# Kernel optimization log

Measured on AMD Instinct MI355X. Metric: run time of the kernel, lower is better.

## Reference

```python
import jax, jax.numpy as jnp
import numpy as np

B, T, N, IN, H, P = 1, 48, 4096, 2, 64, 12


def _normalize_adj(adj):
    A = adj + jnp.eye(adj.shape[0], dtype=adj.dtype)
    d = jnp.sum(A, axis=1)
    dinv = jnp.where(d > 0, d ** -0.5, 0.0)
    return (dinv[:, None] * A) * dinv[None, :]


def _cell(inp, h, c, A, gcWi, gcbi, gcWh, gcbh, liWi, libi, liWh, libh):
    # graph conv: spmm(A, inp @ W) + bias, plus plain linears; all produce [BN, 4H]
    comb = (A @ (inp @ gcWi) + gcbi
            + A @ (h @ gcWh) + gcbh
            + inp @ liWi + libi
            + h @ liWh + libh)
    i_g, f_g, o_g, g_g = jnp.split(comb, 4, axis=1)
    new_c = jax.nn.sigmoid(f_g) * c + jax.nn.sigmoid(i_g) * jnp.tanh(g_g)
    new_h = jax.nn.sigmoid(o_g) * jnp.tanh(new_c)
    return new_h, new_c


def setup_inputs() -> dict:
    key = jax.random.key(0)
    ks = jax.random.split(key, 24)
    s_in = 1.0 / np.sqrt(4 * H)

    def p(k, shape):
        return jax.random.normal(k, shape, dtype=jnp.float32) * s_in

    adj = (jax.random.uniform(ks[1], (N, N)) < 0.01).astype(jnp.float32)
    return {
        "x": jax.random.normal(ks[0], (B, T, N * IN), dtype=jnp.float32),
        "adj": adj,
        "gcWi0": p(ks[2], (IN, 4 * H)), "gcbi0": p(ks[3], (4 * H,)),
        "gcWh0": p(ks[4], (H, 4 * H)), "gcbh0": p(ks[5], (4 * H,)),
        "liWi0": p(ks[6], (IN, 4 * H)), "libi0": p(ks[7], (4 * H,)),
        "liWh0": p(ks[8], (H, 4 * H)), "libh0": p(ks[9], (4 * H,)),
        "gcWi1": p(ks[10], (H, 4 * H)), "gcbi1": p(ks[11], (4 * H,)),
        "gcWh1": p(ks[12], (H, 4 * H)), "gcbh1": p(ks[13], (4 * H,)),
        "liWi1": p(ks[14], (H, 4 * H)), "libi1": p(ks[15], (4 * H,)),
        "liWh1": p(ks[16], (H, 4 * H)), "libh1": p(ks[17], (4 * H,)),
        "outW": p(ks[18], (H, P)), "outb": p(ks[19], (P,)),
    }


def reference(x, adj, gcWi0, gcbi0, gcWh0, gcbh0, liWi0, libi0, liWh0, libh0,
              gcWi1, gcbi1, gcWh1, gcbh1, liWi1, libi1, liWh1, libh1, outW, outb):
    A = _normalize_adj(adj)
    # [B,T,N*IN] -> time-major [T, B*N, IN]
    xs = x.reshape(B, T, N, IN).transpose(1, 0, 2, 3).reshape(T, B * N, IN)
    z = jnp.zeros((B * N, H), dtype=x.dtype)

    def step(carry, xt):
        h0, c0, h1, c1 = carry
        h0, c0 = _cell(xt, h0, c0, A, gcWi0, gcbi0, gcWh0, gcbh0,
                       liWi0, libi0, liWh0, libh0)
        # dropout is identity in eval mode
        h1, c1 = _cell(h0, h1, c1, A, gcWi1, gcbi1, gcWh1, gcbh1,
                       liWi1, libi1, liWh1, libh1)
        return (h0, c0, h1, c1), None

    (h0, c0, h1, c1), _ = jax.lax.scan(step, (z, z, z, z), xs)
    out = h1 @ outW + outb  # [B*N, P]
    return out.reshape(B, N, P)
```

## Files before the change

### kernel.cpp

```cpp
#include <hip/hip_runtime.h>
#include <math.h>

#define NN 4096
#define TT 48
#define HH 64
#define GG 256
#define PP 12
#define CAP 192
#define NH (NN * HH)

__device__ __forceinline__ float bcast_f(float v, int lane) {
  return __int_as_float(__builtin_amdgcn_readlane(__float_as_int(v), lane));
}
__device__ __forceinline__ int bcast_i(int v, int lane) {
  return __builtin_amdgcn_readlane(v, lane);
}

__launch_bounds__(256)
__global__ void k_prep(const float* gcbi0, const float* gcbh0,
                       const float* libi0, const float* libh0,
                       const float* gcbi1, const float* gcbh1,
                       const float* libi1, const float* libh1,
                       const float* gcWh0, const float* liWh0,
                       const float* gcWi1, const float* liWi1,
                       const float* gcWh1, const float* liWh1,
                       const float* gcWi0, const float* liWi0,
                       float* state, float4* Wg0, float4* Wg1,
                       float4* biasg0, float4* biasg1, float4* xq0) {
  int idx = blockIdx.x * 256 + threadIdx.x;
  int stride = gridDim.x * 256;
  for (int i = idx; i < 6 * NH; i += stride) state[i] = 0.0f;
  for (int i = idx; i < 64 * 2 * 64; i += stride) {
    int j = i & 63, m = (i >> 6) & 1, k = i >> 7;
    const float* W = m ? liWh0 : gcWh0;
    Wg0[i] = make_float4(W[k * GG + j], W[k * GG + j + 64],
                         W[k * GG + j + 128], W[k * GG + j + 192]);
  }
  for (int i = idx; i < 64 * 4 * 64; i += stride) {
    int j = i & 63, m = (i >> 6) & 3, k = i >> 8;
    const float* W = (m == 0) ? gcWi1 : (m == 1) ? liWi1 : (m == 2) ? gcWh1 : liWh1;
    Wg1[i] = make_float4(W[k * GG + j], W[k * GG + j + 64],
                         W[k * GG + j + 128], W[k * GG + j + 192]);
  }
  if (idx < 64) {
    int j = idx;
    biasg0[j] = make_float4(
        gcbi0[j] + gcbh0[j] + libi0[j] + libh0[j],
        gcbi0[j + 64] + gcbh0[j + 64] + libi0[j + 64] + libh0[j + 64],
        gcbi0[j + 128] + gcbh0[j + 128] + libi0[j + 128] + libh0[j + 128],
        gcbi0[j + 192] + gcbh0[j + 192] + libi0[j + 192] + libh0[j + 192]);
    biasg1[j] = make_float4(
        gcbi1[j] + gcbh1[j] + libi1[j] + libh1[j],
        gcbi1[j + 64] + gcbh1[j + 64] + libi1[j + 64] + libh1[j + 64],
        gcbi1[j + 128] + gcbh1[j + 128] + libi1[j + 128] + libh1[j + 128],
        gcbi1[j + 192] + gcbh1[j + 192] + libi1[j + 192] + libh1[j + 192]);
  } else if (idx < 320) {
    int i = idx - 64;
    int j = i & 63, m = i >> 6;
    const float* W = (m < 2) ? gcWi0 : liWi0;
    int kk = m & 1;
    xq0[i] = make_float4(W[kk * GG + j], W[kk * GG + j + 64],
                         W[kk * GG + j + 128], W[kk * GG + j + 192]);
  }
}

__launch_bounds__(256)
__global__ void k_build(const float* adj, float* dinv,
                        int* ell_col, float* ell_val, int* ell_cnt) {
  int r = blockIdx.x;
  __shared__ int cnt;
  __shared__ float red[256];
  if (threadIdx.x == 0) cnt = 0;
  __syncthreads();
  const float* row = adj + (size_t)r * NN;
  float s = 0.0f;
  for (int c = threadIdx.x; c < NN; c += 256) {
    float a = row[c];
    if (c == r) a += 1.0f;
    s += a;
    if (a != 0.0f) {
      int pos = atomicAdd(&cnt, 1);
      if (pos < CAP) {
        ell_col[(size_t)r * CAP + pos] = c;
        ell_val[(size_t)r * CAP + pos] = a;
      }
    }
  }
  red[threadIdx.x] = s;
  __syncthreads();
  for (int st = 128; st > 0; st >>= 1) {
    if (threadIdx.x < st) red[threadIdx.x] += red[threadIdx.x + st];
    __syncthreads();
  }
  int n = cnt < CAP ? cnt : CAP;
  for (int j = n + (int)threadIdx.x; j < CAP; j += 256) {
    ell_col[(size_t)r * CAP + j] = 0;
    ell_val[(size_t)r * CAP + j] = 0.0f;
  }
  if (threadIdx.x == 0) {
    int npad = (n + 7) & ~7;
    if (npad > CAP) npad = CAP;
    ell_cnt[r] = npad;
    dinv[r] = 1.0f / sqrtf(red[0]);
  }
}

__launch_bounds__(256)
__global__ void k_scale(const float* dinv, const int* ell_col, float* ell_val) {
  int idx = blockIdx.x * 256 + threadIdx.x;
  int r = idx / CAP;
  if (r >= NN) return;
  float v = ell_val[idx];
  if (v != 0.0f) ell_val[idx] = v * dinv[r] * dinv[ell_col[idx]];
}

__launch_bounds__(256)
__global__ void k_gax(const float* x, const int* ell_col, const float* ell_val,
                      const int* ell_cnt, float* gax) {
  int t = blockIdx.x >> 3;
  int seg = blockIdx.x & 7;
  __shared__ float xs[NN * 2];
  const float* xt = x + (size_t)t * NN * 2;
  for (int i = threadIdx.x; i < NN * 2; i += 256) xs[i] = xt[i];
  __syncthreads();
  int base = seg * 512 * 2;
  for (int oo = threadIdx.x; oo < 512 * 2; oo += 256) {
    int o = base + oo;
    int r = o >> 1, cmp = o & 1;
    int cnt = ell_cnt[r];
    const int* cp = ell_col + (size_t)r * CAP;
    const float* vp = ell_val + (size_t)r * CAP;
    float acc = 0.0f;
    for (int j = 0; j < cnt; j += 4) {
      acc += vp[j]     * xs[cp[j]     * 2 + cmp];
      acc += vp[j + 1] * xs[cp[j + 1] * 2 + cmp];
      acc += vp[j + 2] * xs[cp[j + 2] * 2 + cmp];
      acc += vp[j + 3] * xs[cp[j + 3] * 2 + cmp];
    }
    gax[(size_t)t * NN * 2 + o] = acc;
  }
}

__launch_bounds__(256)
__global__ void k_cells(int c0on, int c1on,
                        const int* __restrict__ ell_col,
                        const float* __restrict__ ell_val,
                        const int* __restrict__ ell_cnt,
                        const float2* __restrict__ Pr, float* __restrict__ Pw,
                        float* __restrict__ c0, float* __restrict__ c1,
                        const float* __restrict__ xt, const float* __restrict__ gaxt,
                        const float4* __restrict__ Wg,
                        const float4* __restrict__ biasg0,
                        const float4* __restrict__ xq0,
                        const float4* __restrict__ biasg1) {
  __shared__ float4 wbuf[2048];
  const int tid = threadIdx.x;
  const int wave = tid >> 6, lane = tid & 63;
  const int r0 = blockIdx.x * 8 + wave * 2;

  const float4* pf = Wg + tid;
  float4 st0 = pf[0], st1 = pf[256], st2 = pf[512], st3 = pf[768];
  pf += 1024;

  float cprev0[2], cprev1[2];
#pragma unroll
  for (int rr = 0; rr < 2; rr++) {
    size_t gi = (size_t)(r0 + rr) * HH + lane;
    cprev0[rr] = c0[gi];
    cprev1[rr] = c1[gi];
  }

  int myc[2][3]; float myv[2][3]; int cnts[2];
#pragma unroll
  for (int rr = 0; rr < 2; rr++) {
    int r = r0 + rr;
    cnts[rr] = ell_cnt[r];
#pragma unroll
    for (int chk = 0; chk < 3; chk++) {
      myc[rr][chk] = ell_col[(size_t)r * CAP + chk * 64 + lane];
      myv[rr][chk] = ell_val[(size_t)r * CAP + chk * 64 + lane];
    }
  }

  float ga0[2], ga1[2], hl0[2], hl1[2];
#pragma unroll
  for (int rr = 0; rr < 2; rr++) {
    int cnt = cnts[rr];
    float a0 = 0.0f, a1 = 0.0f;
#pragma unroll
    for (int chk = 0; chk < 3; chk++) {
      int base = chk * 64;
      if (base < cnt) {
        int lim = cnt - base; if (lim > 64) lim = 64;
        int mc = myc[rr][chk]; float mv = myv[rr][chk];
        for (int m = 0; m < lim; m += 8) {
          float2 ld[8]; float vv[8];
#pragma unroll
          for (int i = 0; i < 8; i++) {
            int cc = bcast_i(mc, m + i);
            vv[i] = bcast_f(mv, m + i);
            ld[i] = Pr[(size_t)cc * 64 + lane];
          }
#pragma unroll
          for (int i = 0; i < 8; i++) {
            a0 += vv[i] * ld[i].x;
            a1 += vv[i] * ld[i].y;
          }
        }
      }
    }
    ga0[rr] = a0;
    ga1[rr] = a1;
    float2 hh = Pr[(size_t)(r0 + rr) * 64 + lane];
    hl0[rr] = hh.x;
    hl1[rr] = hh.y;
  }

  float4 acc0[2], acc1[2];
  {
    float4 b = biasg0[lane];
    float4 qg0 = xq0[lane], qg1 = xq0[64 + lane];
    float4 ql0 = xq0[128 + lane], ql1 = xq0[192 + lane];
#pragma unroll
    for (int rr = 0; rr < 2; rr++) {
      float xx0 = xt[(size_t)(r0 + rr) * 2];
      float xx1 = xt[(size_t)(r0 + rr) * 2 + 1];
      float gg0 = gaxt[(size_t)(r0 + rr) * 2];
      float gg1 = gaxt[(size_t)(r0 + rr) * 2 + 1];
      acc0[rr].x = b.x + gg0 * qg0.x + gg1 * qg1.x + xx0 * ql0.x + xx1 * ql1.x;
      acc0[rr].y = b.y + gg0 * qg0.y + gg1 * qg1.y + xx0 * ql0.y + xx1 * ql1.y;
      acc0[rr].z = b.z + gg0 * qg0.z + gg1 * qg1.z + xx0 * ql0.z + xx1 * ql1.z;
      acc0[rr].w = b.w + gg0 * qg0.w + gg1 * qg1.w + xx0 * ql0.w + xx1 * ql1.w;
    }
    float4 b1 = biasg1[lane];
    acc1[0] = b1; acc1[1] = b1;
  }

  wbuf[tid] = st0; wbuf[256 + tid] = st1;
  wbuf[512 + tid] = st2; wbuf[768 + tid] = st3;
  __syncthreads();
  int cur = 0;

#pragma unroll 1
  for (int ch = 0; ch < 8; ch++) {
    st0 = pf[0]; st1 = pf[256]; st2 = pf[512]; st3 = pf[768];
    pf += 1024;
    const float4* wb = wbuf + (cur << 10);
#pragma unroll
    for (int kk = 0; kk < 8; kk++) {
      int k = ch * 8 + kk;
      float4 w0 = wb[(kk * 2 + 0) * 64 + lane];
      float4 w1 = wb[(kk * 2 + 1) * 64 + lane];
#pragma unroll
      for (int rr = 0; rr < 2; rr++) {
        float a0 = bcast_f(ga0[rr], k);
        float a1 = bcast_f(hl0[rr], k);
        acc0[rr].x += a0 * w0.x + a1 * w1.x;
        acc0[rr].y += a0 * w0.y + a1 * w1.y;
        acc0[rr].z += a0 * w0.z + a1 * w1.z;
        acc0[rr].w += a0 * w0.w + a1 * w1.w;
      }
    }
    cur ^= 1;
    float4* dst = wbuf + (cur << 10) + tid;
    dst[0] = st0; dst[256] = st1; dst[512] = st2; dst[768] = st3;
    __syncthreads();
  }

  if (c0on) {
#pragma unroll
    for (int rr = 0; rr < 2; rr++) {
      size_t gi = (size_t)(r0 + rr) * HH + lane;
      float si = 1.0f / (1.0f + __expf(-acc0[rr].x));
      float sf = 1.0f / (1.0f + __expf(-acc0[rr].y));
      float so = 1.0f / (1.0f + __expf(-acc0[rr].z));
      float cn = sf * cprev0[rr] + si * tanhf(acc0[rr].w);
      float hn = so * tanhf(cn);
      c0[gi] = cn;
      Pw[gi * 2 + 0] = hn;
    }
  }

  if (c1on) {
#pragma unroll 1
    for (int ch = 0; ch < 16; ch++) {
      if (ch + 1 < 16) {
        st0 = pf[0]; st1 = pf[256]; st2 = pf[512]; st3 = pf[768];
        pf += 1024;
      }
      const float4* wb = wbuf + (cur << 10);
#pragma unroll
      for (int kk = 0; kk < 4; kk++) {
        int k = ch * 4 + kk;
        float4 w0 = wb[(kk * 4 + 0) * 64 + lane];
        float4 w1 = wb[(kk * 4 + 1) * 64 + lane];
        float4 w2 = wb[(kk * 4 + 2) * 64 + lane];
        float4 w3 = wb[(kk * 4 + 3) * 64 + lane];
#pragma unroll
        for (int rr = 0; rr < 2; rr++) {
          float a0 = bcast_f(ga0[rr], k);
          float a1 = bcast_f(hl0[rr], k);
          float a2 = bcast_f(ga1[rr], k);
          float a3 = bcast_f(hl1[rr], k);
          acc1[rr].x += a0 * w0.x + a1 * w1.x + a2 * w2.x + a3 * w3.x;
          acc1[rr].y += a0 * w0.y + a1 * w1.y + a2 * w2.y + a3 * w3.y;
          acc1[rr].z += a0 * w0.z + a1 * w1.z + a2 * w2.z + a3 * w3.z;
          acc1[rr].w += a0 * w0.w + a1 * w1.w + a2 * w2.w + a3 * w3.w;
        }
      }
      if (ch + 1 < 16) {
        cur ^= 1;
        float4* dst = wbuf + (cur << 10) + tid;
        dst[0] = st0; dst[256] = st1; dst[512] = st2; dst[768] = st3;
        __syncthreads();
      }
    }
#pragma unroll
    for (int rr = 0; rr < 2; rr++) {
      size_t gi = (size_t)(r0 + rr) * HH + lane;
      float si = 1.0f / (1.0f + __expf(-acc1[rr].x));
      float sf = 1.0f / (1.0f + __expf(-acc1[rr].y));
      float so = 1.0f / (1.0f + __expf(-acc1[rr].z));
      float cn = sf * cprev1[rr] + si * tanhf(acc1[rr].w);
      float hn = so * tanhf(cn);
      c1[gi] = cn;
      Pw[gi * 2 + 1] = hn;
    }
  }
}

__launch_bounds__(256)
__global__ void k_out(const float* __restrict__ P0, const float* __restrict__ outW,
                      const float* __restrict__ outb, float* __restrict__ out) {
  int idx = blockIdx.x * 256 + threadIdx.x;
  if (idx >= NN * PP) return;
  int r = idx / PP, p = idx - r * PP;
  float acc = outb[p];
  const float* hrow = P0 + (size_t)r * 128;
#pragma unroll 16
  for (int k = 0; k < HH; k++) acc += hrow[k * 2 + 1] * outW[k * PP + p];
  out[idx] = acc;
}

extern "C" void kernel_launch(void* const* d_in, const int* in_sizes, int n_in,
                              void* d_out, int out_size, void* d_ws, size_t ws_size,
                              hipStream_t stream) {
  const float* x     = (const float*)d_in[0];
  const float* adj   = (const float*)d_in[1];
  const float* gcWi0 = (const float*)d_in[2];
  const float* gcbi0 = (const float*)d_in[3];
  const float* gcWh0 = (const float*)d_in[4];
  const float* gcbh0 = (const float*)d_in[5];
  const float* liWi0 = (const float*)d_in[6];
  const float* libi0 = (const float*)d_in[7];
  const float* liWh0 = (const float*)d_in[8];
  const float* libh0 = (const float*)d_in[9];
  const float* gcWi1 = (const float*)d_in[10];
  const float* gcbi1 = (const float*)d_in[11];
  const float* gcWh1 = (const float*)d_in[12];
  const float* gcbh1 = (const float*)d_in[13];
  const float* liWi1 = (const float*)d_in[14];
  const float* libi1 = (const float*)d_in[15];
  const float* liWh1 = (const float*)d_in[16];
  const float* libh1 = (const float*)d_in[17];
  const float* outW  = (const float*)d_in[18];
  const float* outb  = (const float*)d_in[19];

  char* ws = (char*)d_ws;
  size_t off = 0;
  auto carve = [&](size_t bytes) {
    void* p = ws + off;
    off += (bytes + 255) & ~(size_t)255;
    return p;
  };
  float*  dinv    = (float*)carve((size_t)NN * 4);
  int*    ell_col = (int*)carve((size_t)NN * CAP * 4);
  float*  ell_val = (float*)carve((size_t)NN * CAP * 4);
  int*    ell_cnt = (int*)carve((size_t)NN * 4);
  float*  state   = (float*)carve((size_t)6 * NH * 4);
  float*  gax     = (float*)carve((size_t)TT * NN * 2 * 4);
  float4* Wgm     = (float4*)carve((size_t)(8192 + 16384) * 16);
  float4* biasg0  = (float4*)carve((size_t)64 * 16);
  float4* biasg1  = (float4*)carve((size_t)64 * 16);
  float4* xq0     = (float4*)carve((size_t)256 * 16);

  float4* Wg0 = Wgm;
  float4* Wg1 = Wgm + 8192;
  float* P[2] = {state, state + 2 * NH};
  float* c0 = state + 4 * NH;
  float* c1 = state + 5 * NH;

  k_prep<<<512, 256, 0, stream>>>(gcbi0, gcbh0, libi0, libh0,
                                  gcbi1, gcbh1, libi1, libh1,
                                  gcWh0, liWh0, gcWi1, liWi1, gcWh1, liWh1,
                                  gcWi0, liWi0,
                                  state, Wg0, Wg1, biasg0, biasg1, xq0);
  k_build<<<NN, 256, 0, stream>>>(adj, dinv, ell_col, ell_val, ell_cnt);
  k_scale<<<(NN * CAP) / 256, 256, 0, stream>>>(dinv, ell_col, ell_val);
  k_gax<<<TT * 8, 256, 0, stream>>>(x, ell_col, ell_val, ell_cnt, gax);

  for (int k = 0; k <= TT; k++) {
    int A = k & 1;
    int c0on = (k < TT) ? 1 : 0;
    int c1on = (k > 0) ? 1 : 0;
    int tx = (k < TT) ? k : (TT - 1);
    k_cells<<<NN / 8, 256, 0, stream>>>(
        c0on, c1on, ell_col, ell_val, ell_cnt,
        (const float2*)P[A ^ 1], P[A], c0, c1,
        x + (size_t)tx * NN * 2, gax + (size_t)tx * NN * 2,
        Wgm, biasg0, xq0, biasg1);
  }

  k_out<<<(NN * PP + 255) / 256, 256, 0, stream>>>(P[0], outW, outb, (float*)d_out);
}
```

Before: 1.797 ms.

## Split k_cells reduction across wave pairs with 512-thread blocks

Doubles the k_cells block to 512 threads. Each row's SpMM gather now runs on one wave instead of two rows per wave, and each wave pair splits the K dimension of both cell matmuls in half, combining partial sums through shared memory. The weight tables are permuted in prep so each half-K slice is laid out contiguously for the staged LDS loads. This aims to raise parallelism and hide latency in the per-step kernel, at the cost of extra LDS traffic, barriers, and computing layer-1 partials even when c1on is off.

```diff
diff --git a/kernel.cpp b/kernel.cpp
--- a/kernel.cpp
+++ b/kernel.cpp
@@ -33,14 +33,18 @@
   for (int i = idx; i < 64 * 2 * 64; i += stride) {
     int j = i & 63, m = (i >> 6) & 1, k = i >> 7;
     const float* W = m ? liWh0 : gcWh0;
-    Wg0[i] = make_float4(W[k * GG + j], W[k * GG + j + 64],
-                         W[k * GG + j + 128], W[k * GG + j + 192]);
+    int slot = ((k & 31) >> 2) * 8 + (k >> 5) * 4 + (k & 3);
+    Wg0[slot * 128 + m * 64 + j] =
+        make_float4(W[k * GG + j], W[k * GG + j + 64],
+                    W[k * GG + j + 128], W[k * GG + j + 192]);
   }
   for (int i = idx; i < 64 * 4 * 64; i += stride) {
     int j = i & 63, m = (i >> 6) & 3, k = i >> 8;
     const float* W = (m == 0) ? gcWi1 : (m == 1) ? liWi1 : (m == 2) ? gcWh1 : liWh1;
-    Wg1[i] = make_float4(W[k * GG + j], W[k * GG + j + 64],
-                         W[k * GG + j + 128], W[k * GG + j + 192]);
+    int slot = ((k & 31) >> 1) * 4 + (k >> 5) * 2 + (k & 1);
+    Wg1[slot * 256 + m * 64 + j] =
+        make_float4(W[k * GG + j], W[k * GG + j + 64],
+                    W[k * GG + j + 128], W[k * GG + j + 192]);
   }
   if (idx < 64) {
     int j = idx;
@@ -141,7 +145,7 @@
   }
 }
 
-__launch_bounds__(256)
+__launch_bounds__(512, 4)
 __global__ void k_cells(int c0on, int c1on,
                         const int* __restrict__ ell_col,
                         const float* __restrict__ ell_val,
@@ -154,70 +158,68 @@
                         const float4* __restrict__ xq0,
                         const float4* __restrict__ biasg1) {
   __shared__ float4 wbuf[2048];
+  __shared__ float4 xbuf[512];
   const int tid = threadIdx.x;
   const int wave = tid >> 6, lane = tid & 63;
-  const int r0 = blockIdx.x * 8 + wave * 2;
+  const int pair = wave >> 1, kh = wave & 1;
+  const int r0 = blockIdx.x * 8 + pair * 2;
+  const int myrow = r0 + kh;
 
   const float4* pf = Wg + tid;
-  float4 st0 = pf[0], st1 = pf[256], st2 = pf[512], st3 = pf[768];
+  float4 st0 = pf[0], st1 = pf[512];
   pf += 1024;
 
-  float cprev0[2], cprev1[2];
+  float cprevA[2];
 #pragma unroll
   for (int rr = 0; rr < 2; rr++) {
     size_t gi = (size_t)(r0 + rr) * HH + lane;
-    cprev0[rr] = c0[gi];
-    cprev1[rr] = c1[gi];
-  }
-
-  int myc[2][3]; float myv[2][3]; int cnts[2];
-#pragma unroll
-  for (int rr = 0; rr < 2; rr++) {
-    int r = r0 + rr;
-    cnts[rr] = ell_cnt[r];
-#pragma unroll
-    for (int chk = 0; chk < 3; chk++) {
-      myc[rr][chk] = ell_col[(size_t)r * CAP + chk * 64 + lane];
-      myv[rr][chk] = ell_val[(size_t)r * CAP + chk * 64 + lane];
-    }
-  }
-
-  float ga0[2], ga1[2], hl0[2], hl1[2];
-#pragma unroll
-  for (int rr = 0; rr < 2; rr++) {
-    int cnt = cnts[rr];
-    float a0 = 0.0f, a1 = 0.0f;
-#pragma unroll
-    for (int chk = 0; chk < 3; chk++) {
-      int base = chk * 64;
-      if (base < cnt) {
-        int lim = cnt - base; if (lim > 64) lim = 64;
-        int mc = myc[rr][chk]; float mv = myv[rr][chk];
-        for (int m = 0; m < lim; m += 8) {
-          float2 ld[8]; float vv[8];
-#pragma unroll
-          for (int i = 0; i < 8; i++) {
-            int cc = bcast_i(mc, m + i);
-            vv[i] = bcast_f(mv, m + i);
-            ld[i] = Pr[(size_t)cc * 64 + lane];
-          }
-#pragma unroll
-          for (int i = 0; i < 8; i++) {
-            a0 += vv[i] * ld[i].x;
-            a1 += vv[i] * ld[i].y;
-          }
+    cprevA[rr] = (kh == 0) ? c0[gi] : c1[gi];
+  }
+
+  int cnt = ell_cnt[myrow];
+  int myc[3]; float myv[3];
+#pragma unroll
+  for (int chk = 0; chk < 3; chk++) {
+    myc[chk] = ell_col[(size_t)myrow * CAP + chk * 64 + lane];
+    myv[chk] = ell_val[(size_t)myrow * CAP + chk * 64 + lane];
+  }
+  float a0 = 0.0f, a1 = 0.0f;
+#pragma unroll
+  for (int chk = 0; chk < 3; chk++) {
+    int base = chk * 64;
+    if (base < cnt) {
+      int lim = cnt - base; if (lim > 64) lim = 64;
+      int mc = myc[chk]; float mv = myv[chk];
+      for (int m = 0; m < lim; m += 8) {
+        float2 ld[8]; float vv[8];
+#pragma unroll
+        for (int i = 0; i < 8; i++) {
+          int cc = bcast_i(mc, m + i);
+          vv[i] = bcast_f(mv, m + i);
+          ld[i] = Pr[(size_t)cc * 64 + lane];
+        }
+#pragma unroll
+        for (int i = 0; i < 8; i++) {
+          a0 += vv[i] * ld[i].x;
+          a1 += vv[i] * ld[i].y;
         }
       }
     }
-    ga0[rr] = a0;
-    ga1[rr] = a1;
+  }
+  {
+    float2* gx = (float2*)xbuf;
+    gx[(size_t)(pair * 2 + kh) * 64 + lane] = make_float2(a0, a1);
+  }
+  float hl0[2], hl1[2];
+#pragma unroll
+  for (int rr = 0; rr < 2; rr++) {
     float2 hh = Pr[(size_t)(r0 + rr) * 64 + lane];
     hl0[rr] = hh.x;
     hl1[rr] = hh.y;
   }
 
   float4 acc0[2], acc1[2];
-  {
+  if (kh == 0) {
     float4 b = biasg0[lane];
     float4 qg0 = xq0[lane], qg1 = xq0[64 + lane];
     float4 ql0 = xq0[128 + lane], ql1 = xq0[192 + lane];
@@ -232,99 +234,134 @@
       acc0[rr].z = b.z + gg0 * qg0.z + gg1 * qg1.z + xx0 * ql0.z + xx1 * ql1.z;
       acc0[rr].w = b.w + gg0 * qg0.w + gg1 * qg1.w + xx0 * ql0.w + xx1 * ql1.w;
     }
+    acc1[0] = make_float4(0.f, 0.f, 0.f, 0.f);
+    acc1[1] = make_float4(0.f, 0.f, 0.f, 0.f);
+  } else {
+    acc0[0] = make_float4(0.f, 0.f, 0.f, 0.f);
+    acc0[1] = make_float4(0.f, 0.f, 0.f, 0.f);
     float4 b1 = biasg1[lane];
     acc1[0] = b1; acc1[1] = b1;
   }
 
-  wbuf[tid] = st0; wbuf[256 + tid] = st1;
-  wbuf[512 + tid] = st2; wbuf[768 + tid] = st3;
+  wbuf[tid] = st0; wbuf[512 + tid] = st1;
   __syncthreads();
+
+  float ga0[2], ga1[2];
+  {
+    const float2* gx = (const float2*)xbuf;
+#pragma unroll
+    for (int rr = 0; rr < 2; rr++) {
+      float2 g = gx[(size_t)(pair * 2 + rr) * 64 + lane];
+      ga0[rr] = g.x;
+      ga1[rr] = g.y;
+    }
+  }
+
   int cur = 0;
-
 #pragma unroll 1
   for (int ch = 0; ch < 8; ch++) {
-    st0 = pf[0]; st1 = pf[256]; st2 = pf[512]; st3 = pf[768];
+    st0 = pf[0]; st1 = pf[512];
     pf += 1024;
     const float4* wb = wbuf + (cur << 10);
-#pragma unroll
-    for (int kk = 0; kk < 8; kk++) {
-      int k = ch * 8 + kk;
-      float4 w0 = wb[(kk * 2 + 0) * 64 + lane];
-      float4 w1 = wb[(kk * 2 + 1) * 64 + lane];
+    const int kb = kh * 32 + ch * 4;
+    const int wbase = kh * 4;
+#pragma unroll
+    for (int q = 0; q < 4; q++) {
+      int k = kb + q;
+      float4 w0 = wb[(wbase + q) * 128 + lane];
+      float4 w1 = wb[(wbase + q) * 128 + 64 + lane];
 #pragma unroll
       for (int rr = 0; rr < 2; rr++) {
-        float a0 = bcast_f(ga0[rr], k);
-        float a1 = bcast_f(hl0[rr], k);
-        acc0[rr].x += a0 * w0.x + a1 * w1.x;
-        acc0[rr].y += a0 * w0.y + a1 * w1.y;
-        acc0[rr].z += a0 * w0.z + a1 * w1.z;
-        acc0[rr].w += a0 * w0.w + a1 * w1.w;
+        float b0 = bcast_f(ga0[rr], k);
+        float b1 = bcast_f(hl0[rr], k);
+        acc0[rr].x += b0 * w0.x + b1 * w1.x;
+        acc0[rr].y += b0 * w0.y + b1 * w1.y;
+        acc0[rr].z += b0 * w0.z + b1 * w1.z;
+        acc0[rr].w += b0 * w0.w + b1 * w1.w;
       }
     }
     cur ^= 1;
     float4* dst = wbuf + (cur << 10) + tid;
-    dst[0] = st0; dst[256] = st1; dst[512] = st2; dst[768] = st3;
+    dst[0] = st0; dst[512] = st1;
+    if (ch == 7 && kh == 1) {
+      xbuf[(size_t)(pair * 2 + 0) * 64 + lane] = acc0[0];
+      xbuf[(size_t)(pair * 2 + 1) * 64 + lane] = acc0[1];
+    }
     __syncthreads();
   }
 
-  if (c0on) {
+  if (c0on && kh == 0) {
 #pragma unroll
     for (int rr = 0; rr < 2; rr++) {
+      float4 o = xbuf[(size_t)(pair * 2 + rr) * 64 + lane];
+      float gxv = acc0[rr].x + o.x, gyv = acc0[rr].y + o.y;
+      float gzv = acc0[rr].z + o.z, gwv = acc0[rr].w + o.w;
       size_t gi = (size_t)(r0 + rr) * HH + lane;
-      float si = 1.0f / (1.0f + __expf(-acc0[rr].x));
-      float sf = 1.0f / (1.0f + __expf(-acc0[rr].y));
-      float so = 1.0f / (1.0f + __expf(-acc0[rr].z));
-      float cn = sf * cprev0[rr] + si * tanhf(acc0[rr].w);
+      float si = 1.0f / (1.0f + __expf(-gxv));
+      float sf = 1.0f / (1.0f + __expf(-gyv));
+      float so = 1.0f / (1.0f + __expf(-gzv));
+      float cn = sf * cprevA[rr] + si * tanhf(gwv);
       float hn = so * tanhf(cn);
       c0[gi] = cn;
       Pw[gi * 2 + 0] = hn;
     }
   }
 
+#pragma unroll 1
+  for (int ch = 0; ch < 16; ch++) {
+    if (ch + 1 < 16) {
+      st0 = pf[0]; st1 = pf[512];
+      pf += 1024;
+    }
+    const float4* wb = wbuf + (cur << 10);
+    const int kb = kh * 32 + ch * 2;
+    const int wbase = kh * 2;
+#pragma unroll
+    for (int q = 0; q < 2; q++) {
+      int k = kb + q;
+      const float4* wp = wb + (wbase + q) * 256 + lane;
+      float4 w0 = wp[0], w1 = wp[64], w2 = wp[128], w3 = wp[192];
+#pragma unroll
+      for (int rr = 0; rr < 2; rr++) {
+        float b0 = bcast_f(ga0[rr], k);
+        float b1 = bcast_f(hl0[rr], k);
+        float b2 = bcast_f(ga1[rr], k);
+        float b3 = bcast_f(hl1[rr], k);
+        acc1[rr].x += b0 * w0.x + b1 * w1.x + b2 * w2.x + b3 * w3.x;
+        acc1[rr].y += b0 * w0.y + b1 * w1.y + b2 * w2.y + b3 * w3.y;
+        acc1[rr].z += b0 * w0.z + b1 * w1.z + b2 * w2.z + b3 * w3.z;
+        acc1[rr].w += b0 * w0.w + b1 * w1.w + b2 * w2.w + b3 * w3.w;
+      }
+    }
+    if (ch + 1 < 16) {
+      cur ^= 1;
+      float4* dst = wbuf + (cur << 10) + tid;
+      dst[0] = st0; dst[512] = st1;
+      __syncthreads();
+    }
+  }
+
   if (c1on) {
-#pragma unroll 1
-    for (int ch = 0; ch < 16; ch++) {
-      if (ch + 1 < 16) {
-        st0 = pf[0]; st1 = pf[256]; st2 = pf[512]; st3 = pf[768];
-        pf += 1024;
+    if (kh == 0) {
+      xbuf[(size_t)(pair * 2 + 0) * 64 + lane] = acc1[0];
+      xbuf[(size_t)(pair * 2 + 1) * 64 + lane] = acc1[1];
+    }
+    __syncthreads();
+    if (kh == 1) {
+#pragma unroll
+      for (int rr = 0; rr < 2; rr++) {
+        float4 o = xbuf[(size_t)(pair * 2 + rr) * 64 + lane];
+        float gxv = acc1[rr].x + o.x, gyv = acc1[rr].y + o.y;
+        float gzv = acc1[rr].z + o.z, gwv = acc1[rr].w + o.w;
+        size_t gi = (size_t)(r0 + rr) * HH + lane;
+        float si = 1.0f / (1.0f + __expf(-gxv));
+        float sf = 1.0f / (1.0f + __expf(-gyv));
+        float so = 1.0f / (1.0f + __expf(-gzv));
+        float cn = sf * cprevA[rr] + si * tanhf(gwv);
+        float hn = so * tanhf(cn);
+        c1[gi] = cn;
+        Pw[gi * 2 + 1] = hn;
       }
-      const float4* wb = wbuf + (cur << 10);
-#pragma unroll
-      for (int kk = 0; kk < 4; kk++) {
-        int k = ch * 4 + kk;
-        float4 w0 = wb[(kk * 4 + 0) * 64 + lane];
-        float4 w1 = wb[(kk * 4 + 1) * 64 + lane];
-        float4 w2 = wb[(kk * 4 + 2) * 64 + lane];
-        float4 w3 = wb[(kk * 4 + 3) * 64 + lane];
-#pragma unroll
-        for (int rr = 0; rr < 2; rr++) {
-          float a0 = bcast_f(ga0[rr], k);
-          float a1 = bcast_f(hl0[rr], k);
-          float a2 = bcast_f(ga1[rr], k);
-          float a3 = bcast_f(hl1[rr], k);
-          acc1[rr].x += a0 * w0.x + a1 * w1.x + a2 * w2.x + a3 * w3.x;
-          acc1[rr].y += a0 * w0.y + a1 * w1.y + a2 * w2.y + a3 * w3.y;
-          acc1[rr].z += a0 * w0.z + a1 * w1.z + a2 * w2.z + a3 * w3.z;
-          acc1[rr].w += a0 * w0.w + a1 * w1.w + a2 * w2.w + a3 * w3.w;
-        }
-      }
-      if (ch + 1 < 16) {
-        cur ^= 1;
-        float4* dst = wbuf + (cur << 10) + tid;
-        dst[0] = st0; dst[256] = st1; dst[512] = st2; dst[768] = st3;
-        __syncthreads();
-      }
-    }
-#pragma unroll
-    for (int rr = 0; rr < 2; rr++) {
-      size_t gi = (size_t)(r0 + rr) * HH + lane;
-      float si = 1.0f / (1.0f + __expf(-acc1[rr].x));
-      float sf = 1.0f / (1.0f + __expf(-acc1[rr].y));
-      float so = 1.0f / (1.0f + __expf(-acc1[rr].z));
-      float cn = sf * cprev1[rr] + si * tanhf(acc1[rr].w);
-      float hn = so * tanhf(cn);
-      c1[gi] = cn;
-      Pw[gi * 2 + 1] = hn;
     }
   }
 }
@@ -404,7 +441,7 @@
     int c0on = (k < TT) ? 1 : 0;
     int c1on = (k > 0) ? 1 : 0;
     int tx = (k < TT) ? k : (TT - 1);
-    k_cells<<<NN / 8, 256, 0, stream>>>(
+    k_cells<<<NN / 8, 512, 0, stream>>>(
         c0on, c1on, ell_col, ell_val, ell_cnt,
         (const float2*)P[A ^ 1], P[A], c0, c1,
         x + (size_t)tx * NN * 2, gax + (size_t)tx * NN * 2,
```

After: 1.728 ms. 3.9% less time.
